# Optimization experiments

Measured on AMD Instinct MI355X. Metric: run time of the kernel, lower is better.

## Reference

```python
import jax, jax.numpy as jnp
import numpy as np

B, L, DM, NL, ED, NS, DC, RK, CD, Q = 8, 1024, 256, 4, 512, 16, 4, 16, 64, 2


def _ln(x, g, b, eps=1e-5):
    m = x.mean(-1, keepdims=True)
    v = ((x - m) ** 2).mean(-1, keepdims=True)
    return (x - m) / jnp.sqrt(v + eps) * g + b


def setup_inputs() -> dict:
    key = jax.random.key(0)
    ks = jax.random.split(key, 32)
    rn = lambda k, sh, s=0.02: jax.random.normal(k, sh, jnp.float32) * s
    inp = {
        "tokens": jax.random.randint(ks[0], (B, L), 0, Q),
        "T": jax.random.uniform(ks[1], (B,), jnp.float32, 0.5, 2.0),
        "tok_embed": rn(ks[2], (Q, DM)),
        "pos_embed": rn(ks[3], (L, DM)),
        "tw1": rn(ks[4], (1, CD), 0.5),
        "tb1": rn(ks[5], (CD,), 0.1),
        "tw2": rn(ks[6], (CD, CD), 0.1),
        "tb2": rn(ks[7], (CD,), 0.1),
        "ag": jnp.ones((NL, DM), jnp.float32),
        "ab": jnp.zeros((NL, DM), jnp.float32),
        "apw": rn(ks[8], (NL, CD, 2 * DM), 0.01),
        "apb": jnp.zeros((NL, 2 * DM), jnp.float32),
        "in_w": rn(ks[9], (NL, DM, 2 * ED)),
        "conv_w": rn(ks[10], (NL, ED, DC), 0.2),
        "conv_b": jnp.zeros((NL, ED), jnp.float32),
        "xp_w": rn(ks[11], (NL, ED, RK + 2 * NS)),
        "dt_w": rn(ks[12], (NL, RK, ED), 0.1),
        "dt_b": rn(ks[13], (NL, ED), 0.1) - 4.0,  # softplus(~-4) gives small dt
        "A_log": jnp.log(jnp.broadcast_to(jnp.arange(1, NS + 1, dtype=jnp.float32), (NL, ED, NS))),
        "Dp": jnp.ones((NL, ED), jnp.float32),
        "out_w": rn(ks[14], (NL, ED, DM)),
        "fg": jnp.ones((DM,), jnp.float32),
        "fb": jnp.zeros((DM,), jnp.float32),
        "hw": rn(ks[15], (DM, Q)),
        "hb": jnp.zeros((Q,), jnp.float32),
    }
    return inp


def reference(tokens, T, tok_embed, pos_embed, tw1, tb1, tw2, tb2, ag, ab, apw, apb,
              in_w, conv_w, conv_b, xp_w, dt_w, dt_b, A_log, Dp, out_w, fg, fb, hw, hb):
    b, l = tokens.shape
    # shift-right token embedding + positional embedding
    emb = tok_embed[tokens]                                   # [B,L,DM]
    x = jnp.concatenate([jnp.zeros((b, 1, emb.shape[-1]), emb.dtype), emb[:, :-1]], axis=1)
    x = x + pos_embed[:l]
    # temperature conditioning MLP (exact GELU as in torch nn.GELU)
    h = jax.nn.gelu(T[:, None] @ tw1 + tb1, approximate=False)
    cond = h @ tw2 + tb2                                      # [B,CD]

    def comb(e1, e2):
        a1, b1 = e1
        a2, b2 = e2
        return a1 * a2, a2 * b1 + b2

    for i in range(NL):
        # AdaLN: (1 + scale) * LN(x) + shift
        ss = cond @ apw[i] + apb[i]                           # [B,2*DM]
        sc, sh = ss[:, :DM], ss[:, DM:]
        xn = (1.0 + sc[:, None, :]) * _ln(x, ag[i], ab[i]) + sh[:, None, :]
        # MambaBlock
        xz = xn @ in_w[i]                                     # [B,L,2*ED]
        xs, z = xz[..., :ED], xz[..., ED:]
        # causal depthwise conv1d (left-pad d_conv-1)
        xc = jnp.transpose(xs, (0, 2, 1))                     # [B,ED,L]
        xc = jax.lax.conv_general_dilated(xc, conv_w[i][:, None, :], (1,), [(DC - 1, 0)],
                                          feature_group_count=ED)
        xc = xc + conv_b[i][None, :, None]
        xs = jax.nn.silu(jnp.transpose(xc, (0, 2, 1)))        # [B,L,ED]
        # input-dependent SSM params
        xd = xs @ xp_w[i]                                     # [B,L,RK+2*NS]
        dlt = jax.nn.softplus(xd[..., :RK] @ dt_w[i] + dt_b[i])  # [B,L,ED]
        Bm, Cm = xd[..., RK:RK + NS], xd[..., RK + NS:]       # [B,L,NS]
        A = -jnp.exp(A_log[i])                                # [ED,NS]
        dA = jnp.exp(dlt[..., None] * A)                      # [B,L,ED,NS]
        dBx = (dlt * xs)[..., None] * Bm[:, :, None, :]       # [B,L,ED,NS]
        # selective scan: h_t = dA_t * h_{t-1} + dBx_t (parallel associative scan)
        _, hs = jax.lax.associative_scan(comb, (dA, dBx), axis=1)
        y = jnp.einsum('blen,bln->ble', hs, Cm) + Dp[i] * xs
        y = y * jax.nn.silu(z)
        x = x + y @ out_w[i]

    x = _ln(x, fg, fb)
    return x @ hw + hb                                        # [B,L,Q]
```

## Files before the change

kernel.cpp:

```cpp
#include <hip/hip_runtime.h>
#include <hip/hip_bf16.h>
#include <math.h>

#define B_   8
#define L_   1024
#define DM_  256
#define NL_  4
#define ED_  512
#define NS_  16
#define DC_  4
#define RK_  16
#define CD_  64
#define Q_   2

#define SEG_  32
#define SLEN_ 32

typedef __hip_bfloat16 bf16_t;
typedef __attribute__((ext_vector_type(8))) short short8;
typedef __attribute__((ext_vector_type(4))) float floatx4;

__device__ __forceinline__ float geluf(float x) {
    return 0.5f * x * (1.0f + erff(x * 0.70710678118654752f));
}
__device__ __forceinline__ float siluf(float x) {
    return x / (1.0f + __expf(-x));
}
__device__ __forceinline__ float softplus_fast(float x) {
    return (x > 20.0f) ? x : __logf(1.0f + __expf(x));
}
__device__ __forceinline__ float b2f(bf16_t v) { return __bfloat162float(v); }
__device__ __forceinline__ short f2bfbits(float v) {
    return __builtin_bit_cast(short, __float2bfloat16(v));
}

__global__ void k_transpose_all(const float* __restrict__ in_w,
                                const float* __restrict__ xp_w,
                                const float* __restrict__ out_w,
                                bf16_t* __restrict__ in_wT,
                                bf16_t* __restrict__ xp_wT,
                                bf16_t* __restrict__ out_wT) {
    __shared__ float t[32][33];
    int z = blockIdx.z;
    int which = z >> 2, layer = z & 3;
    const float* src; bf16_t* dst; int R, C;
    if (which == 0)      { R = DM_; C = 2 * ED_; src = in_w;  dst = in_wT;  }
    else if (which == 1) { R = ED_; C = 48;      src = xp_w;  dst = xp_wT;  }
    else                 { R = ED_; C = DM_;     src = out_w; dst = out_wT; }
    src += (size_t)layer * R * C;
    dst += (size_t)layer * R * C;
    int c0 = blockIdx.x * 32, r0 = blockIdx.y * 32;
    if (c0 >= C || r0 >= R) return;
    int tx = threadIdx.x & 31, ty = threadIdx.x >> 5;
    #pragma unroll
    for (int i = 0; i < 32; i += 8) {
        int r = r0 + ty + i, c = c0 + tx;
        t[ty + i][tx] = (r < R && c < C) ? src[(size_t)r * C + c] : 0.f;
    }
    __syncthreads();
    #pragma unroll
    for (int i = 0; i < 32; i += 8) {
        int c = c0 + ty + i, r = r0 + tx;
        if (c < C && r < R) dst[(size_t)c * R + r] = __float2bfloat16(t[tx][ty + i]);
    }
}

__global__ void k_embed(const int* __restrict__ tokens,
                        const float* __restrict__ tok_embed,
                        const float* __restrict__ pos_embed,
                        float* __restrict__ x) {
    int row = blockIdx.x;
    int d = threadIdx.x;
    int b = row / L_, l = row % L_;
    float v = pos_embed[l * DM_ + d];
    if (l > 0) {
        int tok = tokens[b * L_ + l - 1];
        v += tok_embed[tok * DM_ + d];
    }
    x[row * DM_ + d] = v;
}

__global__ void k_prep(const float* __restrict__ T,
                       const float* __restrict__ tw1, const float* __restrict__ tb1,
                       const float* __restrict__ tw2, const float* __restrict__ tb2,
                       const float* __restrict__ apw, const float* __restrict__ apb,
                       float* __restrict__ ss) {
    __shared__ float h[CD_], cnd[CD_];
    int b = blockIdx.x, layer = blockIdx.y;
    int j = threadIdx.x;
    if (j < CD_) h[j] = geluf(T[b] * tw1[j] + tb1[j]);
    __syncthreads();
    if (j < CD_) {
        float acc = tb2[j];
        #pragma unroll
        for (int c = 0; c < CD_; c++) acc += h[c] * tw2[c * CD_ + j];
        cnd[j] = acc;
    }
    __syncthreads();
    const float* w = apw + (size_t)layer * CD_ * 2 * DM_;
    float acc = apb[layer * 2 * DM_ + j];
    #pragma unroll
    for (int c = 0; c < CD_; c++) acc += cnd[c] * w[c * 2 * DM_ + j];
    ss[((size_t)layer * B_ + b) * 2 * DM_ + j] = acc;
}

__global__ __launch_bounds__(256) void k_ln_gemm_in(
        const float* __restrict__ x,
        const float* __restrict__ ag, const float* __restrict__ ab,
        const float* __restrict__ ss,
        const bf16_t* __restrict__ Bt,
        bf16_t* __restrict__ xz, int layer) {
    constexpr int BM = 64, BN = 128, K = 256, N = 2 * ED_;
    constexpr int TM = 2, TN = 4;
    __shared__ __align__(16) unsigned short sA[BM * 40];
    __shared__ __align__(16) unsigned short sB[BN * 40];
    __shared__ float s_mr[BM][2];
    __shared__ float s_prm[4 * DM_];

    const int tid = threadIdx.x;
    const int wave = tid >> 6, lane = tid & 63;
    const int lrow = lane & 15, lq = lane >> 4;
    const int bi = blockIdx.x;
    const int row0 = (bi & 127) * BM, col0 = (bi >> 7) * BN;
    const int b = row0 / L_;
    const int wm0 = (wave >> 1) * 32, wn0 = (wave & 1) * 64;

    {
        s_prm[tid]       = ag[layer * DM_ + tid];
        s_prm[256 + tid] = ab[layer * DM_ + tid];
        const float* ssl = ss + ((size_t)layer * B_ + b) * 2 * DM_;
        s_prm[512 + tid] = 1.0f + ssl[tid];
        s_prm[768 + tid] = ssl[DM_ + tid];
    }
    {
        int r = tid >> 2, part = tid & 3;
        const float* xr = x + (size_t)(row0 + r) * K + part * 64;
        float s = 0.f, q = 0.f;
        #pragma unroll
        for (int i = 0; i < 16; i++) {
            float4 v = *(const float4*)(xr + i * 4);
            s += (v.x + v.y) + (v.z + v.w);
            q += (v.x * v.x + v.y * v.y) + (v.z * v.z + v.w * v.w);
        }
        s += __shfl_xor(s, 1, 64);  q += __shfl_xor(q, 1, 64);
        s += __shfl_xor(s, 2, 64);  q += __shfl_xor(q, 2, 64);
        if (part == 0) {
            float mean = s * (1.0f / K);
            float var = q * (1.0f / K) - mean * mean;
            s_mr[r][0] = mean;
            s_mr[r][1] = rsqrtf(var + 1e-5f);
        }
    }

    floatx4 acc[TM][TN];
    #pragma unroll
    for (int i = 0; i < TM; i++)
        #pragma unroll
        for (int j = 0; j < TN; j++) acc[i][j] = (floatx4)0.0f;

    float4 raf[2];
    short8 rb[2];
    const int NKB = K / 32;
    {
        int m = tid >> 2, ko = (tid & 3) * 8;
        raf[0] = *(const float4*)(x + (size_t)(row0 + m) * K + ko);
        raf[1] = *(const float4*)(x + (size_t)(row0 + m) * K + ko + 4);
    }
    #pragma unroll
    for (int i = 0; i < 2; i++) {
        int v = tid + i * 256; int n = v >> 2, ko = (v & 3) * 8;
        rb[i] = *(const short8*)(Bt + (size_t)(col0 + n) * K + ko);
    }

    for (int kb = 0; kb < NKB; kb++) {
        __syncthreads();
        {
            int m = tid >> 2, ko = (tid & 3) * 8;
            int c0 = kb * 32 + ko;
            float mean = s_mr[m][0], rstd = s_mr[m][1];
            float av[8] = {raf[0].x, raf[0].y, raf[0].z, raf[0].w,
                           raf[1].x, raf[1].y, raf[1].z, raf[1].w};
            short8 o;
            #pragma unroll
            for (int j = 0; j < 8; j++) {
                int c = c0 + j;
                float ln = (av[j] - mean) * rstd * s_prm[c] + s_prm[256 + c];
                o[j] = f2bfbits(s_prm[512 + c] * ln + s_prm[768 + c]);
            }
            *(short8*)&sA[m * 40 + ko] = o;
        }
        #pragma unroll
        for (int i = 0; i < 2; i++) {
            int v = tid + i * 256; int n = v >> 2, ko = (v & 3) * 8;
            *(short8*)&sB[n * 40 + ko] = rb[i];
        }
        __syncthreads();
        if (kb + 1 < NKB) {
            int k0 = (kb + 1) * 32;
            {
                int m = tid >> 2, ko = (tid & 3) * 8;
                raf[0] = *(const float4*)(x + (size_t)(row0 + m) * K + k0 + ko);
                raf[1] = *(const float4*)(x + (size_t)(row0 + m) * K + k0 + ko + 4);
            }
            #pragma unroll
            for (int i = 0; i < 2; i++) {
                int v = tid + i * 256; int n = v >> 2, ko = (v & 3) * 8;
                rb[i] = *(const short8*)(Bt + (size_t)(col0 + n) * K + k0 + ko);
            }
        }
        short8 af[TM], bfr[TN];
        #pragma unroll
        for (int i = 0; i < TM; i++)
            af[i] = *(const short8*)&sA[(wm0 + i * 16 + lrow) * 40 + lq * 8];
        #pragma unroll
        for (int j = 0; j < TN; j++)
            bfr[j] = *(const short8*)&sB[(wn0 + j * 16 + lrow) * 40 + lq * 8];
        #pragma unroll
        for (int i = 0; i < TM; i++)
            #pragma unroll
            for (int j = 0; j < TN; j++)
                acc[i][j] = __builtin_amdgcn_mfma_f32_16x16x32_bf16(af[i], bfr[j], acc[i][j], 0, 0, 0);
    }

    #pragma unroll
    for (int i = 0; i < TM; i++) {
        int gr0 = row0 + wm0 + i * 16 + lq * 4;
        #pragma unroll
        for (int j = 0; j < TN; j++) {
            int gc = col0 + wn0 + j * 16 + lrow;
            #pragma unroll
            for (int r = 0; r < 4; r++) {
                float val = acc[i][j][r];
                if (gc >= ED_) val = siluf(val);
                xz[(size_t)(gr0 + r) * N + gc] = __float2bfloat16(val);
            }
        }
    }
}

__global__ __launch_bounds__(256) void k_conv_xp_dlt(
        const bf16_t* __restrict__ xz,
        const float* __restrict__ conv_w, const float* __restrict__ conv_b,
        const bf16_t* __restrict__ Bt,
        bf16_t* __restrict__ xs,
        float* __restrict__ xd,
        const float* __restrict__ dt_w, const float* __restrict__ dt_b,
        bf16_t* __restrict__ dlt, int layer) {
    constexpr int K = ED_;
    constexpr int BM = 16;
    __shared__ __align__(16) unsigned short sA[BM][520];
    __shared__ __align__(16) float s_rk[BM][20];

    const int tid = threadIdx.x;
    const int wave = tid >> 6, lane = tid & 63;
    const int lrow = lane & 15, lq = lane >> 4;
    const int row0 = blockIdx.x * BM;
    const int b = row0 >> 10;
    const int l0 = row0 & (L_ - 1);

    {
        const int e0 = tid * 2;
        float4 w0 = *(const float4*)(conv_w + ((size_t)layer * ED_ + e0) * DC_);
        float4 w1 = *(const float4*)(conv_w + ((size_t)layer * ED_ + e0 + 1) * DC_);
        float bias0 = conv_b[layer * ED_ + e0];
        float bias1 = conv_b[layer * ED_ + e0 + 1];
        const float wa0[4] = {w0.x, w0.y, w0.z, w0.w};
        const float wa1[4] = {w1.x, w1.y, w1.z, w1.w};
        float v0[BM + 3], v1[BM + 3];
        #pragma unroll
        for (int k = 0; k < BM + 3; k++) {
            int ll = l0 - 3 + k;
            if (ll >= 0) {
                __hip_bfloat162 v = *(const __hip_bfloat162*)(
                    xz + ((size_t)(b * L_ + ll)) * (2 * ED_) + e0);
                v0[k] = b2f(v.x); v1[k] = b2f(v.y);
            } else { v0[k] = 0.f; v1[k] = 0.f; }
        }
        #pragma unroll
        for (int j = 0; j < BM; j++) {
            float a0 = bias0, a1 = bias1;
            #pragma unroll
            for (int k = 0; k < DC_; k++) {
                a0 = fmaf(v0[j + k], wa0[k], a0);
                a1 = fmaf(v1[j + k], wa1[k], a1);
            }
            __hip_bfloat162 o;
            o.x = __float2bfloat16(siluf(a0));
            o.y = __float2bfloat16(siluf(a1));
            *(__hip_bfloat162*)(xs + (size_t)(row0 + j) * ED_ + e0) = o;
            *(__hip_bfloat162*)&sA[j][e0] = o;
        }
    }
    __syncthreads();

    const int nrow = (wave < 3) ? (wave * 16 + lrow) : lrow;
    const bf16_t* bptr = Bt + (size_t)nrow * K + lq * 8;
    floatx4 acc = (floatx4)0.0f;
    #pragma unroll
    for (int kb = 0; kb < K / 32; kb++) {
        short8 af = *(const short8*)&sA[lrow][kb * 32 + lq * 8];
        short8 bf = *(const short8*)(bptr + kb * 32);
        acc = __builtin_amdgcn_mfma_f32_16x16x32_bf16(af, bf, acc, 0, 0, 0);
    }

    if (wave == 1 || wave == 2) {
        int gc = wave * 16 + lrow;
        #pragma unroll
        for (int r = 0; r < 4; r++) {
            int gr = row0 + lq * 4 + r;
            xd[(size_t)gr * 48 + gc] = acc[r];
        }
    }
    if (wave == 0) {
        #pragma unroll
        for (int r = 0; r < 4; r++)
            s_rk[lq * 4 + r][lrow] = acc[r];
    }
    __syncthreads();

    const int e = 2 * tid;
    float2 wv[16];
    #pragma unroll
    for (int r = 0; r < RK_; r++)
        wv[r] = *(const float2*)(dt_w + ((size_t)layer * RK_ + r) * ED_ + e);
    float2 bb = *(const float2*)(dt_b + (size_t)layer * ED_ + e);
    #pragma unroll 4
    for (int row = 0; row < BM; row++) {
        float rk[16];
        #pragma unroll
        for (int q = 0; q < 4; q++)
            *(float4*)&rk[q * 4] = *(const float4*)&s_rk[row][q * 4];
        float a0 = bb.x, a1 = bb.y;
        #pragma unroll
        for (int r = 0; r < RK_; r++) {
            a0 = fmaf(rk[r], wv[r].x, a0);
            a1 = fmaf(rk[r], wv[r].y, a1);
        }
        __hip_bfloat162 o;
        o.x = __float2bfloat16(softplus_fast(a0));
        o.y = __float2bfloat16(softplus_fast(a1));
        *(__hip_bfloat162*)(dlt + (size_t)(row0 + row) * ED_ + e) = o;
    }
}


__global__ __launch_bounds__(256) void k_scan1(
        const bf16_t* __restrict__ dlt, const bf16_t* __restrict__ xs,
        const float* __restrict__ xd,
        const float* __restrict__ A_log,
        float* __restrict__ aprod, float* __restrict__ hend, int layer) {
    __shared__ float s_B[SLEN_][16];
    const int te = threadIdx.x;
    const int bi = blockIdx.x;
    const int seg = bi & (SEG_ - 1);
    const int eh  = (bi >> 5) & 1;
    const int b   = bi >> 6;
    const int e   = eh * 256 + te;
    const int rowbase = b * L_ + seg * SLEN_;

    if (te < SLEN_ * 4) {
        int flat = te * 4;
        int r = flat >> 4, c = flat & 15;
        *(float4*)&s_B[r][c] = *(const float4*)(xd + (size_t)(rowbase + r) * 48 + 16 + c);
    }

    float A[16];
    bool geo = true;
    {
        const float* ap = A_log + ((size_t)layer * ED_ + e) * NS_;
        #pragma unroll
        for (int n = 0; n < 16; n++) A[n] = -__expf(ap[n]);
        #pragma unroll
        for (int n = 1; n < 16; n++)
            geo = geo && (fabsf(A[n] - (float)(n + 1) * A[0]) <= 1e-3f * (float)(n + 1) * fabsf(A[0]));
    }

    float h[16];
    #pragma unroll
    for (int n = 0; n < 16; n++) h[n] = 0.f;
    float Pr = 1.0f;
    float P[16];
    #pragma unroll
    for (int n = 0; n < 16; n++) P[n] = 1.f;

    const bf16_t* dptr = dlt + (size_t)rowbase * ED_ + e;
    const bf16_t* xptr = xs  + (size_t)rowbase * ED_ + e;

    bf16_t dvb[8], xvb[8];
    #pragma unroll
    for (int j = 0; j < 8; j++) {
        dvb[j] = dptr[(size_t)j * ED_];
        xvb[j] = xptr[(size_t)j * ED_];
    }
    __syncthreads();

    for (int sub = 0; sub < SLEN_ / 8; sub++) {
        bf16_t dnx[8], xnx[8];
        if (sub < SLEN_ / 8 - 1) {
            const bf16_t* d2 = dptr + (size_t)(sub + 1) * 8 * ED_;
            const bf16_t* x2 = xptr + (size_t)(sub + 1) * 8 * ED_;
            #pragma unroll
            for (int j = 0; j < 8; j++) {
                dnx[j] = d2[(size_t)j * ED_];
                xnx[j] = x2[(size_t)j * ED_];
            }
        }
        if (geo) {
            #pragma unroll
            for (int j = 0; j < 8; j++) {
                int l = sub * 8 + j;
                float dv = b2f(dvb[j]), xv = b2f(xvb[j]);
                float dx = dv * xv;
                float Bv[16];
                #pragma unroll
                for (int q = 0; q < 4; q++)
                    *(float4*)&Bv[q * 4] = *(const float4*)&s_B[l][q * 4];
                float r = __expf(dv * A[0]);
                float r2 = r * r, r4 = r2 * r2;
                float a0 = r, a1 = r2, a2 = r2 * r, a3 = r4;
                #pragma unroll
                for (int q = 0; q < 4; q++) {
                    h[4*q+0] = fmaf(a0, h[4*q+0], dx * Bv[4*q+0]);
                    h[4*q+1] = fmaf(a1, h[4*q+1], dx * Bv[4*q+1]);
                    h[4*q+2] = fmaf(a2, h[4*q+2], dx * Bv[4*q+2]);
                    h[4*q+3] = fmaf(a3, h[4*q+3], dx * Bv[4*q+3]);
                    if (q < 3) { a0 *= r4; a1 *= r4; a2 *= r4; a3 *= r4; }
                }
                Pr *= r;
            }
        } else {
            #pragma unroll
            for (int j = 0; j < 8; j++) {
                int l = sub * 8 + j;
                float dv = b2f(dvb[j]), xv = b2f(xvb[j]);
                float dx = dv * xv;
                float Bv[16];
                #pragma unroll
                for (int q = 0; q < 4; q++)
                    *(float4*)&Bv[q * 4] = *(const float4*)&s_B[l][q * 4];
                #pragma unroll
                for (int n = 0; n < 16; n++) {
                    float a = __expf(dv * A[n]);
                    h[n] = fmaf(a, h[n], dx * Bv[n]);
                    P[n] *= a;
                }
            }
        }
        #pragma unroll
        for (int j = 0; j < 8; j++) { dvb[j] = dnx[j]; xvb[j] = xnx[j]; }
    }

    if (geo) {
        float p = Pr;
        #pragma unroll
        for (int n = 0; n < 16; n++) { P[n] = p; p *= Pr; }
    }
    #pragma unroll
    for (int n = 0; n < 16; n++) {
        size_t idx = ((((size_t)b * SEG_ + seg) << 4) + n) * ED_ + e;
        aprod[idx] = P[n];
        hend[idx]  = h[n];
    }
}

__global__ __launch_bounds__(256) void k_hinit(
        const float* __restrict__ aprod, const float* __restrict__ hend,
        float* __restrict__ hinit) {
    const int te = threadIdx.x;
    const int bi = blockIdx.x;
    const int n  = bi & 15;
    const int eh = (bi >> 4) & 1;
    const int b  = bi >> 5;
    const int e  = eh * 256 + te;
    float h = 0.f;
    for (int s = 0; s < SEG_; s++) {
        size_t idx = ((((size_t)b * SEG_ + s) << 4) + n) * ED_ + e;
        hinit[idx] = h;
        h = fmaf(aprod[idx], h, hend[idx]);
    }
}

__global__ __launch_bounds__(512) void k_scan3_out(
        const bf16_t* __restrict__ dlt, const bf16_t* __restrict__ xs,
        const float* __restrict__ xd,
        const bf16_t* __restrict__ xz,
        const float* __restrict__ A_log, const float* __restrict__ Dp,
        const float* __restrict__ hinit,
        const bf16_t* __restrict__ Bt,
        float* __restrict__ x, int layer) {
    __shared__ float s_BC[SLEN_][32];
    __shared__ __align__(16) unsigned short sy[SLEN_][520];
    const int te = threadIdx.x;
    const int bi = blockIdx.x;
    const int seg = bi & (SEG_ - 1);
    const int b   = bi >> 5;
    const int e   = te;
    const int rowbase = b * L_ + seg * SLEN_;

    {
        int flat = te * 2;
        int r = flat >> 5, c = flat & 31;
        *(float2*)&s_BC[r][c] = *(const float2*)(xd + (size_t)(rowbase + r) * 48 + 16 + c);
    }

    float A[16];
    bool geo = true;
    {
        const float* ap = A_log + ((size_t)layer * ED_ + e) * NS_;
        #pragma unroll
        for (int n = 0; n < 16; n++) A[n] = -__expf(ap[n]);
        #pragma unroll
        for (int n = 1; n < 16; n++)
            geo = geo && (fabsf(A[n] - (float)(n + 1) * A[0]) <= 1e-3f * (float)(n + 1) * fabsf(A[0]));
    }
    const float D = Dp[layer * ED_ + e];

    float h[16];
    {
        const size_t hb = (((size_t)b * SEG_ + seg) << 4) * ED_ + e;
        #pragma unroll
        for (int n = 0; n < 16; n++) h[n] = hinit[hb + (size_t)n * ED_];
    }

    const bf16_t* dptr = dlt + (size_t)rowbase * ED_ + e;
    const bf16_t* xptr = xs  + (size_t)rowbase * ED_ + e;
    const bf16_t* zptr = xz  + (size_t)rowbase * (2 * ED_) + ED_ + e;

    bf16_t dvb[8], xvb[8], zvb[8];
    #pragma unroll
    for (int j = 0; j < 8; j++) {
        dvb[j] = dptr[(size_t)j * ED_];
        xvb[j] = xptr[(size_t)j * ED_];
        zvb[j] = zptr[(size_t)j * (2 * ED_)];
    }
    __syncthreads();

    for (int sub = 0; sub < SLEN_ / 8; sub++) {
        bf16_t dnx[8], xnx[8], znx[8];
        if (sub < SLEN_ / 8 - 1) {
            const bf16_t* d2 = dptr + (size_t)(sub + 1) * 8 * ED_;
            const bf16_t* x2 = xptr + (size_t)(sub + 1) * 8 * ED_;
            const bf16_t* z2 = zptr + (size_t)(sub + 1) * 8 * (2 * ED_);
            #pragma unroll
            for (int j = 0; j < 8; j++) {
                dnx[j] = d2[(size_t)j * ED_];
                xnx[j] = x2[(size_t)j * ED_];
                znx[j] = z2[(size_t)j * (2 * ED_)];
            }
        }
        if (geo) {
            #pragma unroll
            for (int j = 0; j < 8; j++) {
                int l = sub * 8 + j;
                float dv = b2f(dvb[j]), xv = b2f(xvb[j]);
                float dx = dv * xv;
                float Bv[16], Cv[16];
                #pragma unroll
                for (int q = 0; q < 4; q++) {
                    *(float4*)&Bv[q * 4] = *(const float4*)&s_BC[l][q * 4];
                    *(float4*)&Cv[q * 4] = *(const float4*)&s_BC[l][16 + q * 4];
                }
                float r = __expf(dv * A[0]);
                float r2 = r * r, r4 = r2 * r2;
                float a0 = r, a1 = r2, a2 = r2 * r, a3 = r4;
                float y0 = D * xv, y1 = 0.f, y2 = 0.f, y3 = 0.f;
                #pragma unroll
                for (int q = 0; q < 4; q++) {
                    h[4*q+0] = fmaf(a0, h[4*q+0], dx * Bv[4*q+0]);
                    h[4*q+1] = fmaf(a1, h[4*q+1], dx * Bv[4*q+1]);
                    h[4*q+2] = fmaf(a2, h[4*q+2], dx * Bv[4*q+2]);
                    h[4*q+3] = fmaf(a3, h[4*q+3], dx * Bv[4*q+3]);
                    y0 = fmaf(Cv[4*q+0], h[4*q+0], y0);
                    y1 = fmaf(Cv[4*q+1], h[4*q+1], y1);
                    y2 = fmaf(Cv[4*q+2], h[4*q+2], y2);
                    y3 = fmaf(Cv[4*q+3], h[4*q+3], y3);
                    if (q < 3) { a0 *= r4; a1 *= r4; a2 *= r4; a3 *= r4; }
                }
                float yv = (y0 + y1) + (y2 + y3);
                sy[l][e] = (unsigned short)f2bfbits(yv * b2f(zvb[j]));
            }
        } else {
            #pragma unroll
            for (int j = 0; j < 8; j++) {
                int l = sub * 8 + j;
                float dv = b2f(dvb[j]), xv = b2f(xvb[j]);
                float dx = dv * xv;
                float Bv[16], Cv[16];
                #pragma unroll
                for (int q = 0; q < 4; q++) {
                    *(float4*)&Bv[q * 4] = *(const float4*)&s_BC[l][q * 4];
                    *(float4*)&Cv[q * 4] = *(const float4*)&s_BC[l][16 + q * 4];
                }
                float y0 = D * xv, y1 = 0.f, y2 = 0.f, y3 = 0.f;
                #pragma unroll
                for (int n = 0; n < 16; n++) {
                    float a = __expf(dv * A[n]);
                    h[n] = fmaf(a, h[n], dx * Bv[n]);
                    float t = Cv[n] * h[n];
                    if ((n & 3) == 0) y0 += t;
                    else if ((n & 3) == 1) y1 += t;
                    else if ((n & 3) == 2) y2 += t;
                    else y3 += t;
                }
                float yv = (y0 + y1) + (y2 + y3);
                sy[l][e] = (unsigned short)f2bfbits(yv * b2f(zvb[j]));
            }
        }
        #pragma unroll
        for (int j = 0; j < 8; j++) { dvb[j] = dnx[j]; xvb[j] = xnx[j]; zvb[j] = znx[j]; }
    }
    __syncthreads();

    {
        const int wave = te >> 6, lane = te & 63;
        const int lrow = lane & 15, lq = lane >> 4;
        const int mt = wave & 1;
        const int ct = wave >> 1;
        floatx4 acc[4];
        #pragma unroll
        for (int t = 0; t < 4; t++) acc[t] = (floatx4)0.0f;
        #pragma unroll 4
        for (int kb = 0; kb < ED_ / 32; kb++) {
            short8 af = *(const short8*)&sy[mt * 16 + lrow][kb * 32 + lq * 8];
            #pragma unroll
            for (int t = 0; t < 4; t++) {
                short8 bf = *(const short8*)(
                    Bt + (size_t)(ct * 64 + t * 16 + lrow) * ED_ + kb * 32 + lq * 8);
                acc[t] = __builtin_amdgcn_mfma_f32_16x16x32_bf16(af, bf, acc[t], 0, 0, 0);
            }
        }
        #pragma unroll
        for (int t = 0; t < 4; t++) {
            int gc = ct * 64 + t * 16 + lrow;
            #pragma unroll
            for (int r = 0; r < 4; r++) {
                int gr = rowbase + mt * 16 + lq * 4 + r;
                x[(size_t)gr * DM_ + gc] += acc[t][r];
            }
        }
    }
}

__global__ void k_final(const float* __restrict__ x,
                        const float* __restrict__ fg, const float* __restrict__ fb,
                        const float* __restrict__ hw, const float* __restrict__ hb,
                        float* __restrict__ out) {
    int lane = threadIdx.x & 63, w = threadIdx.x >> 6;
    int row = blockIdx.x * 4 + w;
    const float* xr = x + (size_t)row * DM_;
    float v[4];
    #pragma unroll
    for (int k = 0; k < 4; k++) v[k] = xr[lane + 64 * k];
    float s = (v[0] + v[1]) + (v[2] + v[3]);
    float q = (v[0] * v[0] + v[1] * v[1]) + (v[2] * v[2] + v[3] * v[3]);
    #pragma unroll
    for (int off = 32; off > 0; off >>= 1) {
        s += __shfl_xor(s, off, 64);
        q += __shfl_xor(q, off, 64);
    }
    float mean = s * (1.0f / DM_);
    float var = q * (1.0f / DM_) - mean * mean;
    float rstd = rsqrtf(var + 1e-5f);
    float s0 = 0.f, s1 = 0.f;
    #pragma unroll
    for (int k = 0; k < 4; k++) {
        int c = lane + 64 * k;
        float xf = (v[k] - mean) * rstd * fg[c] + fb[c];
        s0 += xf * hw[c * Q_ + 0];
        s1 += xf * hw[c * Q_ + 1];
    }
    #pragma unroll
    for (int off = 32; off > 0; off >>= 1) {
        s0 += __shfl_xor(s0, off, 64);
        s1 += __shfl_xor(s1, off, 64);
    }
    if (lane == 0) {
        out[row * Q_ + 0] = s0 + hb[0];
        out[row * Q_ + 1] = s1 + hb[1];
    }
}

extern "C" void kernel_launch(void* const* d_in, const int* in_sizes, int n_in,
                              void* d_out, int out_size, void* d_ws, size_t ws_size,
                              hipStream_t stream) {
    const int*   tokens    = (const int*)d_in[0];
    const float* T         = (const float*)d_in[1];
    const float* tok_embed = (const float*)d_in[2];
    const float* pos_embed = (const float*)d_in[3];
    const float* tw1       = (const float*)d_in[4];
    const float* tb1       = (const float*)d_in[5];
    const float* tw2       = (const float*)d_in[6];
    const float* tb2       = (const float*)d_in[7];
    const float* ag        = (const float*)d_in[8];
    const float* ab        = (const float*)d_in[9];
    const float* apw       = (const float*)d_in[10];
    const float* apb       = (const float*)d_in[11];
    const float* in_w      = (const float*)d_in[12];
    const float* conv_w    = (const float*)d_in[13];
    const float* conv_b    = (const float*)d_in[14];
    const float* xp_w      = (const float*)d_in[15];
    const float* dt_w      = (const float*)d_in[16];
    const float* dt_b      = (const float*)d_in[17];
    const float* A_log     = (const float*)d_in[18];
    const float* Dp        = (const float*)d_in[19];
    const float* out_w     = (const float*)d_in[20];
    const float* fg        = (const float*)d_in[21];
    const float* fb        = (const float*)d_in[22];
    const float* hw        = (const float*)d_in[23];
    const float* hb        = (const float*)d_in[24];
    float* out = (float*)d_out;

    const int ROWS = B_ * L_;

    char* p = (char*)d_ws;
    float*  x      = (float*)p;   p += (size_t)ROWS * DM_ * 4;
    bf16_t* xz     = (bf16_t*)p;  p += (size_t)ROWS * 2 * ED_ * 2;
    bf16_t* xs     = (bf16_t*)p;  p += (size_t)ROWS * ED_ * 2;
    float*  xd     = (float*)p;   p += (size_t)ROWS * 48 * 4;
    bf16_t* dlt    = (bf16_t*)p;  p += (size_t)ROWS * ED_ * 2;
    float*  ss     = (float*)p;   p += (size_t)NL_ * B_ * 2 * DM_ * 4;
    float*  aprod  = (float*)p;   p += (size_t)B_ * SEG_ * NS_ * ED_ * 4;
    float*  hendb  = (float*)p;   p += (size_t)B_ * SEG_ * NS_ * ED_ * 4;
    float*  hinit  = (float*)p;   p += (size_t)B_ * SEG_ * NS_ * ED_ * 4;
    bf16_t* in_wT  = (bf16_t*)p;  p += (size_t)NL_ * 2 * ED_ * DM_ * 2;
    bf16_t* xp_wT  = (bf16_t*)p;  p += (size_t)NL_ * 48 * ED_ * 2;
    bf16_t* out_wT = (bf16_t*)p;  p += (size_t)NL_ * DM_ * ED_ * 2;

    k_transpose_all<<<dim3(32, 16, 12), 256, 0, stream>>>(
        in_w, xp_w, out_w, in_wT, xp_wT, out_wT);
    k_prep<<<dim3(B_, NL_), 2 * DM_, 0, stream>>>(T, tw1, tb1, tw2, tb2, apw, apb, ss);
    k_embed<<<ROWS, DM_, 0, stream>>>(tokens, tok_embed, pos_embed, x);

    for (int i = 0; i < NL_; i++) {
        k_ln_gemm_in<<<1024, 256, 0, stream>>>(
            x, ag, ab, ss, in_wT + (size_t)i * 2 * ED_ * DM_, xz, i);
        k_conv_xp_dlt<<<ROWS / 16, 256, 0, stream>>>(
            xz, conv_w, conv_b, xp_wT + (size_t)i * 48 * ED_, xs, xd,
            dt_w, dt_b, dlt, i);
        k_scan1<<<B_ * 2 * SEG_, 256, 0, stream>>>(dlt, xs, xd, A_log, aprod, hendb, i);
        k_hinit<<<B_ * 2 * NS_, 256, 0, stream>>>(aprod, hendb, hinit);
        k_scan3_out<<<B_ * SEG_, 512, 0, stream>>>(
            dlt, xs, xd, xz, A_log, Dp, hinit,
            out_wT + (size_t)i * DM_ * ED_, x, i);
    }

    k_final<<<ROWS / 4, 256, 0, stream>>>(x, fg, fb, hw, hb, out);
}
```

Baseline: 455.4 us.

## Fuse conv/x_proj/dt kernel with first scan pass per 32-row segment

Merges the conv+x_proj+dt-projection kernel with the segment-local scan (scan1), so each 512-thread block handles one 32-step segment of one batch across all channels. The block keeps xs in shared memory, dt in registers and B in shared memory, so scan1 no longer re-reads dlt, xs and xd from global memory, and one launch per layer goes away. In exchange the grid shrinks from 512 blocks to 256 larger blocks, which lowers parallelism. Register pressure also rises from the 32-entry dlt array plus the scan state.

```diff
diff --git a/kernel.cpp b/kernel.cpp
--- a/kernel.cpp
+++ b/kernel.cpp
@@ -30,6 +30,9 @@
     return (x > 20.0f) ? x : __logf(1.0f + __expf(x));
 }
 __device__ __forceinline__ float b2f(bf16_t v) { return __bfloat162float(v); }
+__device__ __forceinline__ float bits2f(unsigned short u) {
+    return __uint_as_float(((unsigned)u) << 16);
+}
 __device__ __forceinline__ short f2bfbits(float v) {
     return __builtin_bit_cast(short, __float2bfloat16(v));
 }
@@ -238,38 +241,43 @@
     }
 }
 
-__global__ __launch_bounds__(256) void k_conv_xp_dlt(
+__global__ __launch_bounds__(512) void k_conv_xp_scan1(
         const bf16_t* __restrict__ xz,
         const float* __restrict__ conv_w, const float* __restrict__ conv_b,
         const bf16_t* __restrict__ Bt,
         bf16_t* __restrict__ xs,
         float* __restrict__ xd,
         const float* __restrict__ dt_w, const float* __restrict__ dt_b,
-        bf16_t* __restrict__ dlt, int layer) {
+        bf16_t* __restrict__ dlt,
+        const float* __restrict__ A_log,
+        float* __restrict__ aprod, float* __restrict__ hend, int layer) {
     constexpr int K = ED_;
-    constexpr int BM = 16;
-    __shared__ __align__(16) unsigned short sA[BM][520];
-    __shared__ __align__(16) float s_rk[BM][20];
+    __shared__ __align__(16) unsigned short sA[SLEN_][520];
+    __shared__ __align__(16) float s_rk[SLEN_][20];
+    __shared__ __align__(16) float s_Bc[SLEN_][16];
 
     const int tid = threadIdx.x;
-    const int wave = tid >> 6, lane = tid & 63;
-    const int lrow = lane & 15, lq = lane >> 4;
-    const int row0 = blockIdx.x * BM;
-    const int b = row0 >> 10;
-    const int l0 = row0 & (L_ - 1);
-
-    {
-        const int e0 = tid * 2;
+    const int bi = blockIdx.x;
+    const int seg = bi & (SEG_ - 1);
+    const int b   = bi >> 5;
+    const int l0  = seg * SLEN_;
+    const int rowbase = b * L_ + l0;
+
+    {
+        const int half = tid >> 8;
+        const int t8   = tid & 255;
+        const int e0   = t8 * 2;
+        const int rb   = half * 16;
         float4 w0 = *(const float4*)(conv_w + ((size_t)layer * ED_ + e0) * DC_);
         float4 w1 = *(const float4*)(conv_w + ((size_t)layer * ED_ + e0 + 1) * DC_);
         float bias0 = conv_b[layer * ED_ + e0];
         float bias1 = conv_b[layer * ED_ + e0 + 1];
         const float wa0[4] = {w0.x, w0.y, w0.z, w0.w};
         const float wa1[4] = {w1.x, w1.y, w1.z, w1.w};
-        float v0[BM + 3], v1[BM + 3];
-        #pragma unroll
-        for (int k = 0; k < BM + 3; k++) {
-            int ll = l0 - 3 + k;
+        float v0[19], v1[19];
+        #pragma unroll
+        for (int k = 0; k < 19; k++) {
+            int ll = l0 + rb - 3 + k;
             if (ll >= 0) {
                 __hip_bfloat162 v = *(const __hip_bfloat162*)(
                     xz + ((size_t)(b * L_ + ll)) * (2 * ED_) + e0);
@@ -277,7 +285,7 @@
             } else { v0[k] = 0.f; v1[k] = 0.f; }
         }
         #pragma unroll
-        for (int j = 0; j < BM; j++) {
+        for (int j = 0; j < 16; j++) {
             float a0 = bias0, a1 = bias1;
             #pragma unroll
             for (int k = 0; k < DC_; k++) {
@@ -287,81 +295,65 @@
             __hip_bfloat162 o;
             o.x = __float2bfloat16(siluf(a0));
             o.y = __float2bfloat16(siluf(a1));
-            *(__hip_bfloat162*)(xs + (size_t)(row0 + j) * ED_ + e0) = o;
-            *(__hip_bfloat162*)&sA[j][e0] = o;
+            *(__hip_bfloat162*)(xs + (size_t)(rowbase + rb + j) * ED_ + e0) = o;
+            *(__hip_bfloat162*)&sA[rb + j][e0] = o;
         }
     }
     __syncthreads();
 
-    const int nrow = (wave < 3) ? (wave * 16 + lrow) : lrow;
-    const bf16_t* bptr = Bt + (size_t)nrow * K + lq * 8;
-    floatx4 acc = (floatx4)0.0f;
-    #pragma unroll
-    for (int kb = 0; kb < K / 32; kb++) {
-        short8 af = *(const short8*)&sA[lrow][kb * 32 + lq * 8];
-        short8 bf = *(const short8*)(bptr + kb * 32);
-        acc = __builtin_amdgcn_mfma_f32_16x16x32_bf16(af, bf, acc, 0, 0, 0);
-    }
-
-    if (wave == 1 || wave == 2) {
-        int gc = wave * 16 + lrow;
-        #pragma unroll
-        for (int r = 0; r < 4; r++) {
-            int gr = row0 + lq * 4 + r;
-            xd[(size_t)gr * 48 + gc] = acc[r];
-        }
-    }
-    if (wave == 0) {
-        #pragma unroll
-        for (int r = 0; r < 4; r++)
-            s_rk[lq * 4 + r][lrow] = acc[r];
+    {
+        const int wave = tid >> 6, lane = tid & 63;
+        const int lrow = lane & 15, lq = lane >> 4;
+        const int mt = wave & 1;
+        const int ct = wave >> 1;
+        const int nrow = (ct < 3) ? ct * 16 + lrow : lrow;
+        const bf16_t* bptr = Bt + (size_t)nrow * K + lq * 8;
+        floatx4 acc = (floatx4)0.0f;
+        #pragma unroll
+        for (int kb = 0; kb < K / 32; kb++) {
+            short8 af = *(const short8*)&sA[mt * 16 + lrow][kb * 32 + lq * 8];
+            short8 bf = *(const short8*)(bptr + kb * 32);
+            acc = __builtin_amdgcn_mfma_f32_16x16x32_bf16(af, bf, acc, 0, 0, 0);
+        }
+        if (ct == 1 || ct == 2) {
+            int gc = ct * 16 + lrow;
+            #pragma unroll
+            for (int r = 0; r < 4; r++) {
+                int lr = mt * 16 + lq * 4 + r;
+                xd[(size_t)(rowbase + lr) * 48 + gc] = acc[r];
+                if (ct == 1) s_Bc[lr][lrow] = acc[r];
+            }
+        }
+        if (ct == 0) {
+            #pragma unroll
+            for (int r = 0; r < 4; r++)
+                s_rk[mt * 16 + lq * 4 + r][lrow] = acc[r];
+        }
     }
     __syncthreads();
 
-    const int e = 2 * tid;
-    float2 wv[16];
-    #pragma unroll
-    for (int r = 0; r < RK_; r++)
-        wv[r] = *(const float2*)(dt_w + ((size_t)layer * RK_ + r) * ED_ + e);
-    float2 bb = *(const float2*)(dt_b + (size_t)layer * ED_ + e);
-    #pragma unroll 4
-    for (int row = 0; row < BM; row++) {
-        float rk[16];
-        #pragma unroll
-        for (int q = 0; q < 4; q++)
-            *(float4*)&rk[q * 4] = *(const float4*)&s_rk[row][q * 4];
-        float a0 = bb.x, a1 = bb.y;
-        #pragma unroll
-        for (int r = 0; r < RK_; r++) {
-            a0 = fmaf(rk[r], wv[r].x, a0);
-            a1 = fmaf(rk[r], wv[r].y, a1);
-        }
-        __hip_bfloat162 o;
-        o.x = __float2bfloat16(softplus_fast(a0));
-        o.y = __float2bfloat16(softplus_fast(a1));
-        *(__hip_bfloat162*)(dlt + (size_t)(row0 + row) * ED_ + e) = o;
-    }
-}
-
-
-__global__ __launch_bounds__(256) void k_scan1(
-        const bf16_t* __restrict__ dlt, const bf16_t* __restrict__ xs,
-        const float* __restrict__ xd,
-        const float* __restrict__ A_log,
-        float* __restrict__ aprod, float* __restrict__ hend, int layer) {
-    __shared__ float s_B[SLEN_][16];
-    const int te = threadIdx.x;
-    const int bi = blockIdx.x;
-    const int seg = bi & (SEG_ - 1);
-    const int eh  = (bi >> 5) & 1;
-    const int b   = bi >> 6;
-    const int e   = eh * 256 + te;
-    const int rowbase = b * L_ + seg * SLEN_;
-
-    if (te < SLEN_ * 4) {
-        int flat = te * 4;
-        int r = flat >> 4, c = flat & 15;
-        *(float4*)&s_B[r][c] = *(const float4*)(xd + (size_t)(rowbase + r) * 48 + 16 + c);
+    const int e = tid;
+    unsigned short dltb[SLEN_];
+    {
+        float wv[16];
+        #pragma unroll
+        for (int r = 0; r < RK_; r++)
+            wv[r] = dt_w[((size_t)layer * RK_ + r) * ED_ + e];
+        float bb = dt_b[(size_t)layer * ED_ + e];
+        #pragma unroll 4
+        for (int row = 0; row < SLEN_; row++) {
+            float rk[16];
+            #pragma unroll
+            for (int q = 0; q < 4; q++)
+                *(float4*)&rk[q * 4] = *(const float4*)&s_rk[row][q * 4];
+            float a0 = bb;
+            #pragma unroll
+            for (int r = 0; r < RK_; r++) a0 = fmaf(rk[r], wv[r], a0);
+            unsigned short ub = (unsigned short)f2bfbits(softplus_fast(a0));
+            dltb[row] = ub;
+            dlt[(size_t)(rowbase + row) * ED_ + e] =
+                __builtin_bit_cast(bf16_t, (short)ub);
+        }
     }
 
     float A[16];
@@ -374,7 +366,6 @@
         for (int n = 1; n < 16; n++)
             geo = geo && (fabsf(A[n] - (float)(n + 1) * A[0]) <= 1e-3f * (float)(n + 1) * fabsf(A[0]));
     }
-
     float h[16];
     #pragma unroll
     for (int n = 0; n < 16; n++) h[n] = 0.f;
@@ -383,77 +374,49 @@
     #pragma unroll
     for (int n = 0; n < 16; n++) P[n] = 1.f;
 
-    const bf16_t* dptr = dlt + (size_t)rowbase * ED_ + e;
-    const bf16_t* xptr = xs  + (size_t)rowbase * ED_ + e;
-
-    bf16_t dvb[8], xvb[8];
-    #pragma unroll
-    for (int j = 0; j < 8; j++) {
-        dvb[j] = dptr[(size_t)j * ED_];
-        xvb[j] = xptr[(size_t)j * ED_];
-    }
-    __syncthreads();
-
-    for (int sub = 0; sub < SLEN_ / 8; sub++) {
-        bf16_t dnx[8], xnx[8];
-        if (sub < SLEN_ / 8 - 1) {
-            const bf16_t* d2 = dptr + (size_t)(sub + 1) * 8 * ED_;
-            const bf16_t* x2 = xptr + (size_t)(sub + 1) * 8 * ED_;
-            #pragma unroll
-            for (int j = 0; j < 8; j++) {
-                dnx[j] = d2[(size_t)j * ED_];
-                xnx[j] = x2[(size_t)j * ED_];
-            }
-        }
-        if (geo) {
-            #pragma unroll
-            for (int j = 0; j < 8; j++) {
-                int l = sub * 8 + j;
-                float dv = b2f(dvb[j]), xv = b2f(xvb[j]);
-                float dx = dv * xv;
-                float Bv[16];
-                #pragma unroll
-                for (int q = 0; q < 4; q++)
-                    *(float4*)&Bv[q * 4] = *(const float4*)&s_B[l][q * 4];
-                float r = __expf(dv * A[0]);
-                float r2 = r * r, r4 = r2 * r2;
-                float a0 = r, a1 = r2, a2 = r2 * r, a3 = r4;
-                #pragma unroll
-                for (int q = 0; q < 4; q++) {
-                    h[4*q+0] = fmaf(a0, h[4*q+0], dx * Bv[4*q+0]);
-                    h[4*q+1] = fmaf(a1, h[4*q+1], dx * Bv[4*q+1]);
-                    h[4*q+2] = fmaf(a2, h[4*q+2], dx * Bv[4*q+2]);
-                    h[4*q+3] = fmaf(a3, h[4*q+3], dx * Bv[4*q+3]);
-                    if (q < 3) { a0 *= r4; a1 *= r4; a2 *= r4; a3 *= r4; }
-                }
-                Pr *= r;
-            }
-        } else {
-            #pragma unroll
-            for (int j = 0; j < 8; j++) {
-                int l = sub * 8 + j;
-                float dv = b2f(dvb[j]), xv = b2f(xvb[j]);
-                float dx = dv * xv;
-                float Bv[16];
-                #pragma unroll
-                for (int q = 0; q < 4; q++)
-                    *(float4*)&Bv[q * 4] = *(const float4*)&s_B[l][q * 4];
-                #pragma unroll
-                for (int n = 0; n < 16; n++) {
-                    float a = __expf(dv * A[n]);
-                    h[n] = fmaf(a, h[n], dx * Bv[n]);
-                    P[n] *= a;
-                }
-            }
-        }
-        #pragma unroll
-        for (int j = 0; j < 8; j++) { dvb[j] = dnx[j]; xvb[j] = xnx[j]; }
-    }
-
     if (geo) {
+        #pragma unroll 8
+        for (int j = 0; j < SLEN_; j++) {
+            float dv = bits2f(dltb[j]);
+            float xv = bits2f(sA[j][e]);
+            float dx = dv * xv;
+            float Bv[16];
+            #pragma unroll
+            for (int q = 0; q < 4; q++)
+                *(float4*)&Bv[q * 4] = *(const float4*)&s_Bc[j][q * 4];
+            float r = __expf(dv * A[0]);
+            float r2 = r * r, r4 = r2 * r2;
+            float a0 = r, a1 = r2, a2 = r2 * r, a3 = r4;
+            #pragma unroll
+            for (int q = 0; q < 4; q++) {
+                h[4*q+0] = fmaf(a0, h[4*q+0], dx * Bv[4*q+0]);
+                h[4*q+1] = fmaf(a1, h[4*q+1], dx * Bv[4*q+1]);
+                h[4*q+2] = fmaf(a2, h[4*q+2], dx * Bv[4*q+2]);
+                h[4*q+3] = fmaf(a3, h[4*q+3], dx * Bv[4*q+3]);
+                if (q < 3) { a0 *= r4; a1 *= r4; a2 *= r4; a3 *= r4; }
+            }
+            Pr *= r;
+        }
         float p = Pr;
         #pragma unroll
         for (int n = 0; n < 16; n++) { P[n] = p; p *= Pr; }
+    } else {
+        #pragma unroll 8
+        for (int j = 0; j < SLEN_; j++) {
+            float dv = bits2f(dltb[j]);
+            float xv = bits2f(sA[j][e]);
+            float dx = dv * xv;
+            float Bv[16];
+            #pragma unroll
+            for (int q = 0; q < 4; q++)
+                *(float4*)&Bv[q * 4] = *(const float4*)&s_Bc[j][q * 4];
+            #pragma unroll
+            for (int n = 0; n < 16; n++) {
+                float a = __expf(dv * A[n]);
+                h[n] = fmaf(a, h[n], dx * Bv[n]);
+                P[n] *= a;
+            }
+        }
     }
     #pragma unroll
     for (int n = 0; n < 16; n++) {
@@ -734,10 +697,9 @@
     for (int i = 0; i < NL_; i++) {
         k_ln_gemm_in<<<1024, 256, 0, stream>>>(
             x, ag, ab, ss, in_wT + (size_t)i * 2 * ED_ * DM_, xz, i);
-        k_conv_xp_dlt<<<ROWS / 16, 256, 0, stream>>>(
+        k_conv_xp_scan1<<<B_ * SEG_, 512, 0, stream>>>(
             xz, conv_w, conv_b, xp_wT + (size_t)i * 48 * ED_, xs, xd,
-            dt_w, dt_b, dlt, i);
-        k_scan1<<<B_ * 2 * SEG_, 256, 0, stream>>>(dlt, xs, xd, A_log, aprod, hendb, i);
+            dt_w, dt_b, dlt, A_log, aprod, hendb, i);
         k_hinit<<<B_ * 2 * NS_, 256, 0, stream>>>(aprod, hendb, hinit);
         k_scan3_out<<<B_ * SEG_, 512, 0, stream>>>(
             dlt, xs, xd, xz, A_log, Dp, hinit,
```

Measured after the change: 531.8 us. +16.8%, slower.

## Split scan3/out-proj kernel over ED halves with atomic accumulation

Applied to the files above, without the earlier changes.

The fused scan + output-projection kernel now runs as 512 blocks of 256 threads instead of 256 blocks of 512. Each block handles half of the expanded dimension and computes a partial K=256 out-projection. The partial results are combined into the residual with atomicAdd. This doubles block count to raise occupancy on a GPU with many CUs, at the cost of doubled atomic traffic into x and non-deterministic summation order.

```diff
diff --git a/kernel.cpp b/kernel.cpp
--- a/kernel.cpp
+++ b/kernel.cpp
@@ -480,7 +480,7 @@
     }
 }
 
-__global__ __launch_bounds__(512) void k_scan3_out(
+__global__ __launch_bounds__(256) void k_scan3_outx(
         const bf16_t* __restrict__ dlt, const bf16_t* __restrict__ xs,
         const float* __restrict__ xd,
         const bf16_t* __restrict__ xz,
@@ -489,18 +489,19 @@
         const bf16_t* __restrict__ Bt,
         float* __restrict__ x, int layer) {
     __shared__ float s_BC[SLEN_][32];
-    __shared__ __align__(16) unsigned short sy[SLEN_][520];
+    __shared__ __align__(16) unsigned short sy[SLEN_][264];
     const int te = threadIdx.x;
     const int bi = blockIdx.x;
     const int seg = bi & (SEG_ - 1);
-    const int b   = bi >> 5;
-    const int e   = te;
+    const int eh  = (bi >> 5) & 1;
+    const int b   = bi >> 6;
+    const int e   = eh * 256 + te;
     const int rowbase = b * L_ + seg * SLEN_;
 
     {
-        int flat = te * 2;
+        int flat = te * 4;
         int r = flat >> 5, c = flat & 31;
-        *(float2*)&s_BC[r][c] = *(const float2*)(xd + (size_t)(rowbase + r) * 48 + 16 + c);
+        *(float4*)&s_BC[r][c] = *(const float4*)(xd + (size_t)(rowbase + r) * 48 + 16 + c);
     }
 
     float A[16];
@@ -577,7 +578,7 @@
                     if (q < 3) { a0 *= r4; a1 *= r4; a2 *= r4; a3 *= r4; }
                 }
                 float yv = (y0 + y1) + (y2 + y3);
-                sy[l][e] = (unsigned short)f2bfbits(yv * b2f(zvb[j]));
+                sy[l][te] = (unsigned short)f2bfbits(yv * b2f(zvb[j]));
             }
         } else {
             #pragma unroll
@@ -603,7 +604,7 @@
                     else y3 += t;
                 }
                 float yv = (y0 + y1) + (y2 + y3);
-                sy[l][e] = (unsigned short)f2bfbits(yv * b2f(zvb[j]));
+                sy[l][te] = (unsigned short)f2bfbits(yv * b2f(zvb[j]));
             }
         }
         #pragma unroll
@@ -614,28 +615,34 @@
     {
         const int wave = te >> 6, lane = te & 63;
         const int lrow = lane & 15, lq = lane >> 4;
-        const int mt = wave & 1;
-        const int ct = wave >> 1;
-        floatx4 acc[4];
-        #pragma unroll
-        for (int t = 0; t < 4; t++) acc[t] = (floatx4)0.0f;
-        #pragma unroll 4
-        for (int kb = 0; kb < ED_ / 32; kb++) {
-            short8 af = *(const short8*)&sy[mt * 16 + lrow][kb * 32 + lq * 8];
+        const int ct = wave;
+        floatx4 acc[2][4];
+        #pragma unroll
+        for (int mt = 0; mt < 2; mt++)
+            #pragma unroll
+            for (int t = 0; t < 4; t++) acc[mt][t] = (floatx4)0.0f;
+        #pragma unroll 2
+        for (int kb = 0; kb < 8; kb++) {
+            short8 af0 = *(const short8*)&sy[lrow][kb * 32 + lq * 8];
+            short8 af1 = *(const short8*)&sy[16 + lrow][kb * 32 + lq * 8];
             #pragma unroll
             for (int t = 0; t < 4; t++) {
                 short8 bf = *(const short8*)(
-                    Bt + (size_t)(ct * 64 + t * 16 + lrow) * ED_ + kb * 32 + lq * 8);
-                acc[t] = __builtin_amdgcn_mfma_f32_16x16x32_bf16(af, bf, acc[t], 0, 0, 0);
-            }
-        }
-        #pragma unroll
-        for (int t = 0; t < 4; t++) {
-            int gc = ct * 64 + t * 16 + lrow;
-            #pragma unroll
-            for (int r = 0; r < 4; r++) {
-                int gr = rowbase + mt * 16 + lq * 4 + r;
-                x[(size_t)gr * DM_ + gc] += acc[t][r];
+                    Bt + (size_t)(ct * 64 + t * 16 + lrow) * ED_ + eh * 256 + kb * 32 + lq * 8);
+                acc[0][t] = __builtin_amdgcn_mfma_f32_16x16x32_bf16(af0, bf, acc[0][t], 0, 0, 0);
+                acc[1][t] = __builtin_amdgcn_mfma_f32_16x16x32_bf16(af1, bf, acc[1][t], 0, 0, 0);
+            }
+        }
+        #pragma unroll
+        for (int mt = 0; mt < 2; mt++) {
+            #pragma unroll
+            for (int t = 0; t < 4; t++) {
+                int gc = ct * 64 + t * 16 + lrow;
+                #pragma unroll
+                for (int r = 0; r < 4; r++) {
+                    int gr = rowbase + mt * 16 + lq * 4 + r;
+                    atomicAdd(&x[(size_t)gr * DM_ + gc], acc[mt][t][r]);
+                }
             }
         }
     }
@@ -739,7 +746,7 @@
             dt_w, dt_b, dlt, i);
         k_scan1<<<B_ * 2 * SEG_, 256, 0, stream>>>(dlt, xs, xd, A_log, aprod, hendb, i);
         k_hinit<<<B_ * 2 * NS_, 256, 0, stream>>>(aprod, hendb, hinit);
-        k_scan3_out<<<B_ * SEG_, 512, 0, stream>>>(
+        k_scan3_outx<<<B_ * 2 * SEG_, 256, 0, stream>>>(
             dlt, xs, xd, xz, A_log, Dp, hinit,
             out_wT + (size_t)i * DM_ * ED_, x, i);
     }
```

Result: no change. 449.5 us (-1.3%).
